# Performance work log

Hardware: AMD Instinct MI355X
Metric: run time of the kernel (lower is better)

Reference implementation:

```python
import jax, jax.numpy as jnp
import numpy as np

# ---- static configuration (mirrors C4WithSyscalls __init__/_build_keys) ----
MEM = 16384            # memory_size
OUT = 64               # output_size
NCTX = MEM + 5 + OUT   # context: [memory, PC, SP, BP, AX, OUT_LEN, output]
SCALE = 10.0
GATE_SCALE = 20.0
ADDR_BITS = int(np.ceil(np.log2(NCTX)))   # 15
TYPE_BITS = 5
KDIM = ADDR_BITS + TYPE_BITS
POWERS = jnp.asarray(2 ** np.arange(ADDR_BITS), jnp.int32)

# opcode values for the 15 experts: IMM,LEA,ADD,SUB,MUL,DIV,MOD,SHL,SHR,EQ,NE,LT,GT,LE,GE
OP_VALS = jnp.asarray([1., 2., 9., 10., 11., 12., 13., 14., 15., 3., 4., 5., 6., 7., 8.], jnp.float32)
# binary ops (everything except IMM, LEA) pop the stack: sp += 8
POP_MASK = jnp.asarray([0., 0.] + [1.] * 13, jnp.float32)


def _build_keys():
    addrs = np.arange(NCTX)
    bits = (addrs[:, None] // (2 ** np.arange(ADDR_BITS))) % 2
    addr_keys = (2.0 * bits - 1.0) * SCALE                       # [N, ADDR_BITS]
    type_tags = np.full((NCTX, TYPE_BITS), -SCALE)
    type_tags[MEM, 0] = SCALE      # PC
    type_tags[MEM + 1, 1] = SCALE  # SP
    type_tags[MEM + 2, 2] = SCALE  # BP
    type_tags[MEM + 3, 3] = SCALE  # AX
    type_tags[MEM + 4:, 4] = SCALE  # OUT_LEN + output slots
    return jnp.asarray(np.concatenate([addr_keys, type_tags], 1), jnp.float32)

KEYS = _build_keys()  # [NCTX, KDIM]


def silu_threshold(x, scale=GATE_SCALE):
    d = scale * x
    return (jax.nn.silu(d + 0.5 * scale) - jax.nn.silu(d - 0.5 * scale)) / scale


def eq_gate(a, b, scale=GATE_SCALE):
    diff = a - b
    return silu_threshold(diff + 0.5, scale) * silu_threshold(-diff + 0.5, scale)


def attend(context, addr):
    """Soft-addressed gather: context [B,NCTX], addr [B] float -> (value [B], weights [B,NCTX])."""
    ai = jnp.clip(addr, 0.0, float(NCTX - 1)).astype(jnp.int32)
    bits = (ai[:, None] // POWERS) % 2
    addr_q = (2.0 * bits.astype(jnp.float32) - 1.0) * SCALE                 # [B, ADDR_BITS]
    type_q = jnp.full((addr.shape[0], TYPE_BITS), -SCALE, jnp.float32)      # memory_type tag
    q = jnp.concatenate([addr_q, type_q], axis=1)                           # [B, KDIM]
    scores = jnp.einsum('nd,bd->bn', KEYS, q) / np.sqrt(KDIM)
    w = jax.nn.softmax(scores, axis=1)
    return jnp.einsum('bn,bn->b', w, context), w


def expert_outputs(a, b, imm, bp):
    """a = stack_top, b = ax. Returns [B, 15] new-ax candidates per expert."""
    safeb = jnp.where(jnp.abs(b) < 1e-6, 1e-6, b)
    div = a / safeb
    mod = a - safeb * jnp.floor(div)
    sh = jnp.clip(b, 0.0, 31.0)
    eq = eq_gate(a, b)
    lt = jax.nn.sigmoid(GATE_SCALE * (b - a - 0.5))
    gt = jax.nn.sigmoid(GATE_SCALE * (a - b - 0.5))
    return jnp.stack([
        imm,               # IMM
        bp + imm,          # LEA
        a + b,             # ADD
        a - b,             # SUB
        a * b,             # MUL
        div,               # DIV
        mod,               # MOD
        a * jnp.exp2(sh),  # SHL
        a * jnp.exp2(-sh), # SHR
        eq,                # EQ
        1.0 - eq,          # NE
        lt,                # LT
        gt,                # GT
        1.0 - gt,          # LE
        1.0 - lt,          # GE
    ], axis=-1)


def _forward(memory, output, ax, pc, sp, bp, out_len, num_steps):
    B = memory.shape[0]
    pcf, spf, bpf = pc.astype(jnp.float32), sp.astype(jnp.float32), bp.astype(jnp.float32)
    olf = out_len.astype(jnp.float32)[:, None]

    def step(carry, _):
        pc_, sp_, bp_, ax_, mem_ = carry
        regs = jnp.stack([pc_, sp_, bp_, ax_], axis=1)                    # [B,4]
        context = jnp.concatenate([mem_, regs, olf, output], axis=1)     # [B,NCTX]
        inst, _ = attend(context, pc_)
        imm = jnp.floor(inst / 256.0)
        opcode = inst - imm * 256.0
        stack_top, w_sp = attend(context, sp_)
        gates = eq_gate(opcode[:, None], OP_VALS[None, :])                # [B,15] soft top-1
        outs = expert_outputs(stack_top, ax_, imm, bp_)                   # [B,15]
        gsum = gates.sum(-1)
        new_ax = (gates * outs).sum(-1) + (1.0 - gsum) * ax_              # NoOp default
        pop_g = (gates * POP_MASK).sum(-1)
        new_sp = sp_ + 8.0 * pop_g
        new_pc = pc_ + 8.0
        # soft scatter: write new_ax back at the (soft) stack-top address
        new_mem = mem_ + pop_g[:, None] * w_sp[:, :MEM] * (new_ax[:, None] - mem_)
        return (new_pc, new_sp, bp_, new_ax, new_mem), None

    carry, _ = jax.lax.scan(step, (pcf, spf, bpf, ax, memory), None, length=num_steps)
    return carry[4]  # final memory [B, MEM]


def setup_inputs() -> dict:
    key = jax.random.key(0)
    k = jax.random.split(key, 8)
    B = 1024
    return {
        'memory': jax.random.normal(k[0], (B, MEM), jnp.float32),
        'output': jax.random.normal(k[1], (B, OUT), jnp.float32),
        'ax': jax.random.normal(k[2], (B,), jnp.float32),
        'pc': jax.random.randint(k[3], (B,), 0, MEM, jnp.int32),
        'sp': jax.random.randint(k[4], (B,), 0, MEM, jnp.int32),
        'bp': jax.random.randint(k[5], (B,), 0, MEM, jnp.int32),
        'out_len': jax.random.randint(k[6], (B,), 0, OUT, jnp.int32),
        'num_steps': 16,
    }


def reference(memory, output, ax, pc, sp, bp, out_len, num_steps):
    return _forward(memory, output, ax, pc, sp, bp, out_len, num_steps)
```

## Files before the change

kernel.cpp:

```cpp
#include <hip/hip_runtime.h>
#include <math.h>

#define MEMSZ 16384
#define NCTX  16453

__device__ __forceinline__ float sigmoidf_(float x) {
    return 1.0f / (1.0f + __expf(-x));
}
__device__ __forceinline__ float siluf_(float x) {
    return x * sigmoidf_(x);
}
__device__ __forceinline__ float silu_thr(float x) {
    float d = 20.0f * x;
    return (siluf_(d + 10.0f) - siluf_(d - 10.0f)) * 0.05f;
}
__device__ __forceinline__ float eq_gate_d(float diff) {
    return silu_thr(diff + 0.5f) * silu_thr(0.5f - diff);
}

__global__ void copy_kernel(const float4* __restrict__ src,
                            float4* __restrict__ dst, int n4) {
    int i = blockIdx.x * blockDim.x + threadIdx.x;
    if (i < n4) dst[i] = src[i];
}

__global__ void sim_kernel(float* __restrict__ mem,
                           const float* __restrict__ outp,
                           const float* __restrict__ ax_in,
                           const int* __restrict__ pc_in,
                           const int* __restrict__ sp_in,
                           const int* __restrict__ bp_in,
                           const int* __restrict__ ol_in,
                           const int* __restrict__ nstep,
                           int B) {
    int b = blockIdx.x * blockDim.x + threadIdx.x;
    if (b >= B) return;

    float* __restrict__ mrow = mem + (size_t)b * MEMSZ;
    const float* __restrict__ orow = outp + (size_t)b * 64;

    float pc  = (float)pc_in[b];
    float sp  = (float)sp_in[b];
    float bp  = (float)bp_in[b];
    float ax  = ax_in[b];
    float olf = (float)ol_in[b];
    int   T   = nstep[0];

    const float opv[15] = {1.f, 2.f, 9.f, 10.f, 11.f, 12.f, 13.f, 14.f, 15.f,
                           3.f, 4.f, 5.f, 6.f, 7.f, 8.f};

    for (int t = 0; t < T; ++t) {
        float a1 = fminf(fmaxf(pc, 0.0f), (float)(NCTX - 1));
        int ai = (int)a1;
        float inst;
        if (ai < MEMSZ) {
            inst = mrow[ai];
        } else {
            int r = ai - MEMSZ;
            float cv = (r == 0) ? pc
                     : (r == 1) ? sp
                     : (r == 2) ? bp
                     : (r == 3) ? ax
                     : (r == 4) ? olf
                                : orow[r - 5];
            inst = 0.5f * (cv + mrow[ai - MEMSZ]);
        }
        float imm = floorf(inst * (1.0f / 256.0f));
        float opc = inst - imm * 256.0f;

        float a2 = fminf(fmaxf(sp, 0.0f), (float)(NCTX - 1));
        int si = (int)a2;
        int target = (si < MEMSZ) ? si : (si - MEMSZ);
        float mtv = mrow[target];
        float stv, wfac;
        if (si < MEMSZ) {
            stv = mtv;
            wfac = 1.0f;
        } else {
            int r = si - MEMSZ;
            float cv = (r == 0) ? pc
                     : (r == 1) ? sp
                     : (r == 2) ? bp
                     : (r == 3) ? ax
                     : (r == 4) ? olf
                                : orow[r - 5];
            stv = 0.5f * (cv + mtv);
            wfac = 0.5f;
        }

        float a = stv, bv = ax;
        float safeb = (fabsf(bv) < 1e-6f) ? 1e-6f : bv;
        float dv = a / safeb;
        float md = a - safeb * floorf(dv);
        float sh = fminf(fmaxf(bv, 0.0f), 31.0f);
        float eq = eq_gate_d(a - bv);
        float lt = sigmoidf_(20.0f * (bv - a - 0.5f));
        float gt = sigmoidf_(20.0f * (a - bv - 0.5f));
        float outs[15] = {
            imm,
            bp + imm,
            a + bv,
            a - bv,
            a * bv,
            dv,
            md,
            a * exp2f(sh),
            a * exp2f(-sh),
            eq,
            1.0f - eq,
            lt,
            gt,
            1.0f - gt,
            1.0f - lt
        };

        float gsum = 0.0f, acc = 0.0f, pop = 0.0f;
#pragma unroll
        for (int j = 0; j < 15; ++j) {
            float g = eq_gate_d(opc - opv[j]);
            gsum += g;
            acc += g * outs[j];
            if (j >= 2) pop += g;
        }
        float nax = acc + (1.0f - gsum) * ax;

        mrow[target] = mtv + pop * wfac * (nax - mtv);

        sp = sp + 8.0f * pop;
        pc = pc + 8.0f;
        ax = nax;
    }
}

extern "C" void kernel_launch(void* const* d_in, const int* in_sizes, int n_in,
                              void* d_out, int out_size, void* d_ws, size_t ws_size,
                              hipStream_t stream) {
    const float* memory = (const float*)d_in[0];
    const float* output = (const float*)d_in[1];
    const float* ax     = (const float*)d_in[2];
    const int*   pc     = (const int*)d_in[3];
    const int*   sp     = (const int*)d_in[4];
    const int*   bp     = (const int*)d_in[5];
    const int*   ol     = (const int*)d_in[6];
    const int*   ns     = (const int*)d_in[7];

    int B = in_sizes[0] / MEMSZ;
    int n = B * MEMSZ;
    int n4 = n / 4;

    float* out = (float*)d_out;

    hipLaunchKernelGGL(copy_kernel, dim3((n4 + 255) / 256), dim3(256), 0, stream,
                       (const float4*)memory, (float4*)out, n4);
    hipLaunchKernelGGL(sim_kernel, dim3((B + 255) / 256), dim3(256), 0, stream,
                       out, output, ax, pc, sp, bp, ol, ns, B);
}
```

Before: 169.4 us.

## Overlap memory copy with simulation via write log and scatter apply pass

Fuses the bulk memory copy and the per-row simulation into one launch. Sim threads read from the original input and record their writes in a small per-row log in workspace, and a second kernel scatters the last write per address into the output. On the fast path the sim batches the instruction loads and stack-top loads up front to expose memory-level parallelism, and falls back to a serial log-checking path when aliasing or register reads occur. This removes the copy-then-sim serialisation but adds a launch, more register use and extra control flow.

Result: slower. 281.2 us (+66.0%).

```diff
diff --git a/kernel.cpp b/kernel.cpp
--- a/kernel.cpp
+++ b/kernel.cpp
@@ -3,6 +3,8 @@
 
 #define MEMSZ 16384
 #define NCTX  16453
+#define MAXT  16
+#define LOGCAP 64
 
 __device__ __forceinline__ float sigmoidf_(float x) {
     return 1.0f / (1.0f + __expf(-x));
@@ -18,117 +20,252 @@
     return silu_thr(diff + 0.5f) * silu_thr(0.5f - diff);
 }
 
-__global__ void copy_kernel(const float4* __restrict__ src,
-                            float4* __restrict__ dst, int n4) {
-    int i = blockIdx.x * blockDim.x + threadIdx.x;
-    if (i < n4) dst[i] = src[i];
-}
-
-__global__ void sim_kernel(float* __restrict__ mem,
-                           const float* __restrict__ outp,
-                           const float* __restrict__ ax_in,
-                           const int* __restrict__ pc_in,
-                           const int* __restrict__ sp_in,
-                           const int* __restrict__ bp_in,
-                           const int* __restrict__ ol_in,
-                           const int* __restrict__ nstep,
-                           int B) {
-    int b = blockIdx.x * blockDim.x + threadIdx.x;
-    if (b >= B) return;
-
-    float* __restrict__ mrow = mem + (size_t)b * MEMSZ;
-    const float* __restrict__ orow = outp + (size_t)b * 64;
-
-    float pc  = (float)pc_in[b];
-    float sp  = (float)sp_in[b];
-    float bp  = (float)bp_in[b];
-    float ax  = ax_in[b];
-    float olf = (float)ol_in[b];
-    int   T   = nstep[0];
-
+__device__ __forceinline__ float clipaddr(float x) {
+    return fminf(fmaxf(x, 0.0f), (float)(NCTX - 1));
+}
+
+__device__ __forceinline__ float regval(int r, float pcv, float spv, float bpv,
+                                        float axv, float olf,
+                                        const float* __restrict__ orow) {
+    return (r == 0) ? pcv
+         : (r == 1) ? spv
+         : (r == 2) ? bpv
+         : (r == 3) ? axv
+         : (r == 4) ? olf
+                    : orow[r - 5];
+}
+
+__device__ __forceinline__ float pop_of(float opc) {
     const float opv[15] = {1.f, 2.f, 9.f, 10.f, 11.f, 12.f, 13.f, 14.f, 15.f,
                            3.f, 4.f, 5.f, 6.f, 7.f, 8.f};
-
-    for (int t = 0; t < T; ++t) {
-        float a1 = fminf(fmaxf(pc, 0.0f), (float)(NCTX - 1));
-        int ai = (int)a1;
-        float inst;
-        if (ai < MEMSZ) {
-            inst = mrow[ai];
-        } else {
-            int r = ai - MEMSZ;
-            float cv = (r == 0) ? pc
-                     : (r == 1) ? sp
-                     : (r == 2) ? bp
-                     : (r == 3) ? ax
-                     : (r == 4) ? olf
-                                : orow[r - 5];
-            inst = 0.5f * (cv + mrow[ai - MEMSZ]);
-        }
-        float imm = floorf(inst * (1.0f / 256.0f));
-        float opc = inst - imm * 256.0f;
-
-        float a2 = fminf(fmaxf(sp, 0.0f), (float)(NCTX - 1));
-        int si = (int)a2;
-        int target = (si < MEMSZ) ? si : (si - MEMSZ);
-        float mtv = mrow[target];
-        float stv, wfac;
-        if (si < MEMSZ) {
-            stv = mtv;
-            wfac = 1.0f;
-        } else {
-            int r = si - MEMSZ;
-            float cv = (r == 0) ? pc
-                     : (r == 1) ? sp
-                     : (r == 2) ? bp
-                     : (r == 3) ? ax
-                     : (r == 4) ? olf
-                                : orow[r - 5];
-            stv = 0.5f * (cv + mtv);
-            wfac = 0.5f;
-        }
-
-        float a = stv, bv = ax;
-        float safeb = (fabsf(bv) < 1e-6f) ? 1e-6f : bv;
-        float dv = a / safeb;
-        float md = a - safeb * floorf(dv);
-        float sh = fminf(fmaxf(bv, 0.0f), 31.0f);
-        float eq = eq_gate_d(a - bv);
-        float lt = sigmoidf_(20.0f * (bv - a - 0.5f));
-        float gt = sigmoidf_(20.0f * (a - bv - 0.5f));
-        float outs[15] = {
-            imm,
-            bp + imm,
-            a + bv,
-            a - bv,
-            a * bv,
-            dv,
-            md,
-            a * exp2f(sh),
-            a * exp2f(-sh),
-            eq,
-            1.0f - eq,
-            lt,
-            gt,
-            1.0f - gt,
-            1.0f - lt
-        };
-
-        float gsum = 0.0f, acc = 0.0f, pop = 0.0f;
-#pragma unroll
-        for (int j = 0; j < 15; ++j) {
-            float g = eq_gate_d(opc - opv[j]);
-            gsum += g;
-            acc += g * outs[j];
-            if (j >= 2) pop += g;
-        }
-        float nax = acc + (1.0f - gsum) * ax;
-
-        mrow[target] = mtv + pop * wfac * (nax - mtv);
-
-        sp = sp + 8.0f * pop;
-        pc = pc + 8.0f;
-        ax = nax;
+    float pop = 0.0f;
+#pragma unroll
+    for (int j = 0; j < 15; ++j) {
+        float g = eq_gate_d(opc - opv[j]);
+        if (j >= 2) pop += g;
+    }
+    return pop;
+}
+
+__device__ __forceinline__ float step_update(float stv, float ax, float imm,
+                                             float bp, float opc, float* pop_out) {
+    const float opv[15] = {1.f, 2.f, 9.f, 10.f, 11.f, 12.f, 13.f, 14.f, 15.f,
+                           3.f, 4.f, 5.f, 6.f, 7.f, 8.f};
+    float a = stv, bv = ax;
+    float safeb = (fabsf(bv) < 1e-6f) ? 1e-6f : bv;
+    float dv = a / safeb;
+    float md = a - safeb * floorf(dv);
+    float sh = fminf(fmaxf(bv, 0.0f), 31.0f);
+    float eq = eq_gate_d(a - bv);
+    float lt = sigmoidf_(20.0f * (bv - a - 0.5f));
+    float gt = sigmoidf_(20.0f * (a - bv - 0.5f));
+    float outs[15] = {
+        imm, bp + imm, a + bv, a - bv, a * bv, dv, md,
+        a * exp2f(sh), a * exp2f(-sh),
+        eq, 1.0f - eq, lt, gt, 1.0f - gt, 1.0f - lt
+    };
+    float gsum = 0.0f, acc = 0.0f, pop = 0.0f;
+#pragma unroll
+    for (int j = 0; j < 15; ++j) {
+        float g = eq_gate_d(opc - opv[j]);
+        gsum += g;
+        acc += g * outs[j];
+        if (j >= 2) pop += g;
+    }
+    *pop_out = pop;
+    return acc + (1.0f - gsum) * ax;
+}
+
+__global__ void copy_sim_kernel(const float* __restrict__ mem,
+                                float* __restrict__ out,
+                                const float* __restrict__ outp,
+                                const float* __restrict__ ax_in,
+                                const int* __restrict__ pc_in,
+                                const int* __restrict__ sp_in,
+                                const int* __restrict__ bp_in,
+                                const int* __restrict__ ol_in,
+                                const int* __restrict__ nstep,
+                                int B, int copyBlocks,
+                                int* la, float* lv) {
+    int blk = blockIdx.x;
+    int tid = threadIdx.x;
+
+    if (blk < copyBlocks) {
+        const float4* s = (const float4*)mem;
+        float4* d = (float4*)out;
+        long n4 = (long)B * MEMSZ / 4;
+        long i = (long)blk * 256 + tid;
+        long stride = (long)copyBlocks * 256;
+#pragma unroll
+        for (int k = 0; k < 8; ++k) {
+            long idx = i + (long)k * stride;
+            if (idx < n4) d[idx] = s[idx];
+        }
+        return;
+    }
+
+    int b = (blk - copyBlocks) * blockDim.x + tid;
+    if (b >= B) return;
+
+    const float* __restrict__ mrow = mem + (size_t)b * MEMSZ;
+    const float* __restrict__ orow = outp + (size_t)b * 64;
+    int*   lrow_a = la + (size_t)b * LOGCAP;
+    float* lrow_v = lv + (size_t)b * LOGCAP;
+
+    float pc0 = (float)pc_in[b];
+    float sp0 = (float)sp_in[b];
+    float bp0 = (float)bp_in[b];
+    float ax0 = ax_in[b];
+    float olf = (float)ol_in[b];
+    int T = nstep[0];
+
+    bool slow = (T > MAXT) || (T < 0);
+    float rawv[MAXT];
+    float spA[MAXT];
+    int   tgt[MAXT];
+    float svr[MAXT];
+    float lvv[MAXT];
+
+    if (!slow) {
+#pragma unroll
+        for (int t = 0; t < MAXT; ++t) {
+            if (t < T) {
+                int ai = (int)clipaddr(pc0 + 8.0f * t);
+                int ia = (ai < MEMSZ) ? ai : ai - MEMSZ;
+                rawv[t] = mrow[ia];
+            }
+        }
+        float spc = sp0;
+#pragma unroll
+        for (int t = 0; t < MAXT; ++t) {
+            if (t >= T) break;
+            int ai = (int)clipaddr(pc0 + 8.0f * t);
+            int ia = (ai < MEMSZ) ? ai : ai - MEMSZ;
+#pragma unroll
+            for (int j = 0; j < MAXT; ++j)
+                if (j < t && tgt[j] == ia) slow = true;
+            float inst;
+            if (ai < MEMSZ) {
+                inst = rawv[t];
+            } else {
+                int r = ai - MEMSZ;
+                if (r == 3) slow = true;
+                float cv = regval(r, pc0 + 8.0f * t, spc, bp0, 0.0f, olf, orow);
+                inst = 0.5f * (cv + rawv[t]);
+            }
+            float imm = floorf(inst * (1.0f / 256.0f));
+            float opc = inst - imm * 256.0f;
+            float popv = pop_of(opc);
+            spA[t] = spc;
+            int si = (int)clipaddr(spc);
+            tgt[t] = (si < MEMSZ) ? si : si - MEMSZ;
+            spc = spc + 8.0f * popv;
+        }
+    }
+
+    if (!slow) {
+#pragma unroll
+        for (int t = 0; t < MAXT; ++t)
+            if (t < T) svr[t] = mrow[tgt[t]];
+        float ax = ax0;
+#pragma unroll
+        for (int t = 0; t < MAXT; ++t) {
+            if (t >= T) break;
+            int ai = (int)clipaddr(pc0 + 8.0f * t);
+            float inst;
+            if (ai < MEMSZ) {
+                inst = rawv[t];
+            } else {
+                int r = ai - MEMSZ;
+                float cv = regval(r, pc0 + 8.0f * t, spA[t], bp0, ax, olf, orow);
+                inst = 0.5f * (cv + rawv[t]);
+            }
+            float imm = floorf(inst * (1.0f / 256.0f));
+            float opc = inst - imm * 256.0f;
+            float mtv = svr[t];
+            int tg = tgt[t];
+#pragma unroll
+            for (int j = 0; j < MAXT; ++j)
+                if (j < t && tgt[j] == tg) mtv = lvv[j];
+            int si = (int)clipaddr(spA[t]);
+            float stv, wf;
+            if (si < MEMSZ) {
+                stv = mtv; wf = 1.0f;
+            } else {
+                int r = si - MEMSZ;
+                float cv = regval(r, pc0 + 8.0f * t, spA[t], bp0, ax, olf, orow);
+                stv = 0.5f * (cv + mtv); wf = 0.5f;
+            }
+            float pop;
+            float nax = step_update(stv, ax, imm, bp0, opc, &pop);
+            lvv[t] = mtv + pop * wf * (nax - mtv);
+            ax = nax;
+        }
+#pragma unroll
+        for (int t = 0; t < MAXT; ++t)
+            if (t < T) { lrow_a[t] = tgt[t]; lrow_v[t] = lvv[t]; }
+    } else {
+        float pc = pc0, sp = sp0, ax = ax0;
+        int Tc = (T > LOGCAP) ? LOGCAP : T;
+        for (int t = 0; t < Tc; ++t) {
+            int ai = (int)clipaddr(pc);
+            int ia = (ai < MEMSZ) ? ai : ai - MEMSZ;
+            float v = mrow[ia];
+            for (int j = 0; j < t; ++j)
+                if (lrow_a[j] == ia) v = lrow_v[j];
+            float inst;
+            if (ai < MEMSZ) {
+                inst = v;
+            } else {
+                int r = ai - MEMSZ;
+                float cv = regval(r, pc, sp, bp0, ax, olf, orow);
+                inst = 0.5f * (cv + v);
+            }
+            float imm = floorf(inst * (1.0f / 256.0f));
+            float opc = inst - imm * 256.0f;
+            int si = (int)clipaddr(sp);
+            int tg = (si < MEMSZ) ? si : si - MEMSZ;
+            float mtv = mrow[tg];
+            for (int j = 0; j < t; ++j)
+                if (lrow_a[j] == tg) mtv = lrow_v[j];
+            float stv, wf;
+            if (si < MEMSZ) {
+                stv = mtv; wf = 1.0f;
+            } else {
+                int r = si - MEMSZ;
+                float cv = regval(r, pc, sp, bp0, ax, olf, orow);
+                stv = 0.5f * (cv + mtv); wf = 0.5f;
+            }
+            float pop;
+            float nax = step_update(stv, ax, imm, bp0, opc, &pop);
+            float val = mtv + pop * wf * (nax - mtv);
+            lrow_a[t] = tg;
+            lrow_v[t] = val;
+            sp = sp + 8.0f * pop;
+            pc = pc + 8.0f;
+            ax = nax;
+        }
+    }
+}
+
+__global__ void apply_kernel(float* __restrict__ out,
+                             const int* __restrict__ la,
+                             const float* __restrict__ lv,
+                             const int* __restrict__ nstep, int B) {
+    int row = blockIdx.x;
+    int tid = threadIdx.x;
+    int T = nstep[0];
+    if (T > LOGCAP) T = LOGCAP;
+    __shared__ int sla[LOGCAP];
+    if (tid < LOGCAP) sla[tid] = (tid < T) ? la[(size_t)row * LOGCAP + tid] : -1;
+    __syncthreads();
+    if (tid < T) {
+        int a = sla[tid];
+        bool last = true;
+        for (int j = tid + 1; j < T; ++j)
+            if (sla[j] == a) last = false;
+        if (last)
+            out[(size_t)row * MEMSZ + a] = lv[(size_t)row * LOGCAP + tid];
     }
 }
 
@@ -145,13 +282,17 @@
     const int*   ns     = (const int*)d_in[7];
 
     int B = in_sizes[0] / MEMSZ;
-    int n = B * MEMSZ;
-    int n4 = n / 4;
+    long n4 = (long)B * MEMSZ / 4;
+    int copyBlocks = (int)((n4 + 256 * 8 - 1) / (256 * 8));
+    int simBlocks = (B + 255) / 256;
 
     float* out = (float*)d_out;
-
-    hipLaunchKernelGGL(copy_kernel, dim3((n4 + 255) / 256), dim3(256), 0, stream,
-                       (const float4*)memory, (float4*)out, n4);
-    hipLaunchKernelGGL(sim_kernel, dim3((B + 255) / 256), dim3(256), 0, stream,
-                       out, output, ax, pc, sp, bp, ol, ns, B);
-}
+    int* la = (int*)d_ws;
+    float* lv = (float*)(la + (size_t)B * LOGCAP);
+
+    hipLaunchKernelGGL(copy_sim_kernel, dim3(copyBlocks + simBlocks), dim3(256), 0, stream,
+                       memory, out, output, ax, pc, sp, bp, ol, ns,
+                       B, copyBlocks, la, lv);
+    hipLaunchKernelGGL(apply_kernel, dim3(B), dim3(64), 0, stream,
+                       out, la, lv, ns, B);
+}
```
